# Performance work log

Measured on AMD Instinct MI355X. Metric: run time of the kernel, lower is better.

The kernel has to match this reference:

```python
import jax, jax.numpy as jnp
import numpy as np

# Config mirrors CrossAttentionAudio2T(dim=768, n_head=12, num_frames=16, spec_frames=8,
# attn_all_frame=True, audio_patch=196, time_encoding=False, use_stpos=True)
B, T, N, NA, ST, D, H = 4, 8, 196, 196, 8, 768, 12
HD = D // H
SCALE = HD ** -0.5


def setup_inputs() -> dict:
    key = jax.random.key(0)
    ks = jax.random.split(key, 12)
    r = lambda k, s: jax.random.normal(k, s, dtype=jnp.float32)
    return dict(
        t_x=r(ks[0], (B, T * N, D)),
        audio=r(ks[1], (NA + 2, B * ST, D)),
        vmae_space_pos=SCALE * r(ks[2], (N, D)),
        audio_space_pos=SCALE * r(ks[3], (NA, D)),
        vmae_temporal_pos=SCALE * r(ks[4], (T, D)),
        audio_temporal_pos=SCALE * r(ks[5], (ST, D)),
        q_w=0.02 * r(ks[6], (D, D)),
        q_b=jnp.zeros((D,), jnp.float32),
        kv_w=0.02 * r(ks[7], (2 * D, D)),
        kv_b=jnp.zeros((2 * D,), jnp.float32),
        proj_w=0.02 * r(ks[8], (D, D)),
        proj_b=jnp.zeros((D,), jnp.float32),
    )


def reference(t_x, audio, vmae_space_pos, audio_space_pos, vmae_temporal_pos,
              audio_temporal_pos, q_w, q_b, kv_w, kv_b, proj_w, proj_b):
    # --- video query tokens: add spatial + temporal pos embeds ---
    x = t_x.reshape(B, T, N, D) + vmae_space_pos          # [B,T,N,D] + [N,D]
    x = x.transpose(0, 2, 1, 3) + vmae_temporal_pos       # [B,N,T,D] + [T,D]
    x = x.transpose(0, 2, 1, 3).reshape(B, T * N, D)      # 'b n t d -> b (t n) d'

    # --- audio key/value tokens: drop 2 lead tokens, add pos embeds ---
    a = audio[2:].reshape(NA, B, ST, D).transpose(1, 2, 0, 3)  # 'n (b t) d -> b t n d'
    a = a + audio_space_pos                                    # [B,ST,NA,D] + [NA,D]
    a = a.transpose(0, 2, 1, 3) + audio_temporal_pos           # [B,NA,ST,D] + [ST,D]
    a = a.reshape(B, NA * ST, D)                               # 'b n t d -> b (n t) d'

    # --- projections ---
    q = (x @ q_w.T + q_b).reshape(B, T * N, H, HD).transpose(0, 2, 1, 3)   # [B,H,Lq,HD]
    kv = (a @ kv_w.T + kv_b).reshape(B, NA * ST, 2, H, HD)
    k = kv[:, :, 0].transpose(0, 2, 1, 3)                                  # [B,H,Lk,HD]
    v = kv[:, :, 1].transpose(0, 2, 1, 3)

    # --- scaled dot-product cross-attention (full score matrix, as in source) ---
    attn = jax.nn.softmax(jnp.einsum('bhqd,bhkd->bhqk', q * SCALE, k), axis=-1)
    o = jnp.einsum('bhqk,bhkd->bhqd', attn, v)
    o = o.transpose(0, 2, 1, 3).reshape(B, T * N, D)
    return o @ proj_w.T + proj_b
```

## Files before the change

### kernel.cpp

```cpp
#include <hip/hip_runtime.h>

typedef short s8v __attribute__((ext_vector_type(8)));
typedef short s4v __attribute__((ext_vector_type(4)));
typedef float f4v __attribute__((ext_vector_type(4)));

#define LQ 1568
#define LK 1568
#define NH 12
#define LQP 1664

__device__ __forceinline__ unsigned short f2bf(float f) {
  union { float f; unsigned u; } x; x.f = f;
  unsigned r = x.u + 0x7FFFu + ((x.u >> 16) & 1u);
  return (unsigned short)(r >> 16);
}
__device__ __forceinline__ float bf2f(unsigned s) {
  union { unsigned u; float f; } x; x.u = s << 16;
  return x.f;
}

__global__ void prep_all(const float* __restrict__ t_x, const float* __restrict__ audio,
                         const float* __restrict__ sp, const float* __restrict__ asp,
                         const float* __restrict__ tp, const float* __restrict__ atp,
                         const float* __restrict__ q_w, const float* __restrict__ kv_w,
                         const float* __restrict__ proj_w,
                         unsigned short* __restrict__ xb, unsigned short* __restrict__ ab,
                         unsigned short* __restrict__ wq, unsigned short* __restrict__ wkv,
                         unsigned short* __restrict__ wp, int total4) {
  const int n1 = 768 * 768 / 4, n2 = 1536 * 768 / 4;
  const int nconv = 2 * n1 + n2;
  int i = blockIdx.x * 256 + threadIdx.x;
  if (i < nconv) {
    const float* src; unsigned short* dst; int j = i;
    if (i < n1)           { src = q_w;    dst = wq;  }
    else if (i < n1 + n2) { src = kv_w;   dst = wkv; j = i - n1; }
    else                  { src = proj_w; dst = wp;  j = i - n1 - n2; }
    float4 v = *(const float4*)(src + (size_t)j * 4);
    ushort4 o;
    o.x = f2bf(v.x); o.y = f2bf(v.y); o.z = f2bf(v.z); o.w = f2bf(v.w);
    *(ushort4*)(dst + (size_t)j * 4) = o;
    return;
  }
  i -= nconv;
  if (i >= 2 * total4) return;
  if (i < total4) {
    int d4 = (i % 192) * 4;
    int row = i / 192;
    int l = row % LQ;
    int t = l / 196, n = l % 196;
    float4 a  = *(const float4*)(t_x + (size_t)i * 4);
    float4 s  = *(const float4*)(sp + n * 768 + d4);
    float4 tt = *(const float4*)(tp + t * 768 + d4);
    ushort4 o;
    o.x = f2bf(a.x + s.x + tt.x);
    o.y = f2bf(a.y + s.y + tt.y);
    o.z = f2bf(a.z + s.z + tt.z);
    o.w = f2bf(a.w + s.w + tt.w);
    *(ushort4*)(xb + (size_t)i * 4) = o;
  } else {
    i -= total4;
    int d4 = (i % 192) * 4;
    int row = i / 192;
    int b = row / LK;
    int r2 = row % LK;
    int na = r2 >> 3, ta = r2 & 7;
    const float* src = audio + ((size_t)(2 + na) * 32 + b * 8 + ta) * 768 + d4;
    float4 a  = *(const float4*)src;
    float4 s  = *(const float4*)(asp + na * 768 + d4);
    float4 tt = *(const float4*)(atp + ta * 768 + d4);
    ushort4 o;
    o.x = f2bf(a.x + s.x + tt.x);
    o.y = f2bf(a.y + s.y + tt.y);
    o.z = f2bf(a.z + s.z + tt.z);
    o.w = f2bf(a.w + s.w + tt.w);
    *(ushort4*)(ab + (size_t)i * 4) = o;
  }
}

__global__ __launch_bounds__(256, 4) void gemm_qkv(
    const unsigned short* __restrict__ xb, const unsigned short* __restrict__ ab,
    const unsigned short* __restrict__ wq, const unsigned short* __restrict__ wkv,
    const float* __restrict__ q_b, const float* __restrict__ kv_b,
    unsigned short* __restrict__ Qs, unsigned short* __restrict__ Kb,
    unsigned short* __restrict__ Vb) {
  __shared__ __align__(16) unsigned short sm[128 * 136];
  unsigned short* As = sm;
  unsigned short* Bs = sm + 8192;
  const int tid = threadIdx.x;
  const int lane = tid & 63, wave = tid >> 6;
  const int wm = wave & 1, wn = wave >> 1;
  const int l15 = lane & 15, quad = lane >> 4;
  const int lr = tid >> 3, lc = (tid & 7) * 8;
  const int row0 = blockIdx.x * 128;
  const int y = blockIdx.y;
  const bool isQ = (y < 6);
  const int col0 = (isQ ? y : y - 6) * 128;
  const unsigned short* A = isQ ? xb : ab;
  const unsigned short* W = isQ ? wq : wkv;
  const float* bias = isQ ? q_b : kv_b;

  f4v acc[4][4] = {};
  for (int k0 = 0; k0 < 768; k0 += 64) {
    __syncthreads();
#pragma unroll
    for (int it = 0; it < 4; ++it) {
      int row = lr + it * 32;
      __builtin_amdgcn_global_load_lds(
          (const __attribute__((address_space(1))) unsigned int*)(A + (size_t)(row0 + row) * 768 + k0 + lc),
          (__attribute__((address_space(3))) unsigned int*)(As + row * 64 + lc), 16, 0, 0);
      __builtin_amdgcn_global_load_lds(
          (const __attribute__((address_space(1))) unsigned int*)(W + (size_t)(col0 + row) * 768 + k0 + lc),
          (__attribute__((address_space(3))) unsigned int*)(Bs + row * 64 + lc), 16, 0, 0);
    }
    __syncthreads();
#pragma unroll
    for (int kk = 0; kk < 2; ++kk) {
      s8v af[4], bf[4];
#pragma unroll
      for (int i = 0; i < 4; ++i) {
        af[i] = *(const s8v*)(As + (wm * 64 + i * 16 + l15) * 64 + kk * 32 + quad * 8);
        bf[i] = *(const s8v*)(Bs + (wn * 64 + i * 16 + l15) * 64 + kk * 32 + quad * 8);
      }
#pragma unroll
      for (int mi = 0; mi < 4; ++mi)
#pragma unroll
        for (int ni = 0; ni < 4; ++ni)
          acc[mi][ni] = __builtin_amdgcn_mfma_f32_16x16x32_bf16(af[mi], bf[ni],
                                                               acc[mi][ni], 0, 0, 0);
    }
  }

  if (!isQ && col0 >= 768) {
#pragma unroll
    for (int mi = 0; mi < 4; ++mi) {
      int rowg = row0 + wm * 64 + mi * 16 + quad * 4;
#pragma unroll
      for (int ni = 0; ni < 4; ++ni) {
        int colg = col0 + wn * 64 + ni * 16 + l15;
        float bv = bias[colg];
        int oo = colg - 768;
        int h = oo >> 6, hd = oo & 63;
        int b = rowg / LK, l0 = rowg - b * LK;
        ushort4 pk;
        pk.x = f2bf(acc[mi][ni][0] + bv);
        pk.y = f2bf(acc[mi][ni][1] + bv);
        pk.z = f2bf(acc[mi][ni][2] + bv);
        pk.w = f2bf(acc[mi][ni][3] + bv);
        *(ushort4*)(Vb + ((((size_t)b * NH + h) * 392 + (l0 >> 2)) * 64 + hd) * 4) = pk;
      }
    }
    return;
  }

  const float sc = isQ ? 0.18033688011112042f : 1.0f;
  __syncthreads();
#pragma unroll
  for (int mi = 0; mi < 4; ++mi) {
    int rl = wm * 64 + mi * 16 + quad * 4;
#pragma unroll
    for (int ni = 0; ni < 4; ++ni) {
      int cl = wn * 64 + ni * 16 + l15;
      float bv = bias[col0 + cl];
#pragma unroll
      for (int r = 0; r < 4; ++r)
        sm[(rl + r) * 136 + cl] = f2bf((acc[mi][ni][r] + bv) * sc);
    }
  }
  __syncthreads();
  {
    int row = tid >> 1, half = tid & 1;
    int gl = row0 + row;
    int b = gl / LQ, l = gl - b * LQ;
    const unsigned short* src = sm + row * 136 + half * 64;
    unsigned short* dst;
    if (isQ) {
      dst = Qs + (((size_t)b * NH + (col0 >> 6) + half) * LQ + l) * 64;
    } else {
      int h = (col0 >> 6) + half;
      int tile = l / 112, rr = l - tile * 112;
      dst = Kb + (((size_t)b * NH + h) * 14 + tile) * 8064 + rr * 72;
    }
#pragma unroll
    for (int j = 0; j < 8; ++j)
      *(uint4*)(dst + j * 8) = *(const uint4*)(src + j * 8);
  }
}

__global__ __launch_bounds__(256, 4) void gemm_proj(
    const unsigned short* __restrict__ A, const unsigned short* __restrict__ W,
    const float* __restrict__ bias, float* __restrict__ out) {
  __shared__ __align__(16) unsigned short As[64 * 64];
  __shared__ __align__(16) unsigned short Bs[128 * 64];
  const int tid = threadIdx.x;
  const int lane = tid & 63, wave = tid >> 6;
  const int wm = wave & 1, wn = wave >> 1;
  const int l15 = lane & 15, quad = lane >> 4;
  const int row0 = blockIdx.x * 64;
  const int col0 = blockIdx.y * 128;
  const int lr = tid >> 3, lc = (tid & 7) * 8;

  f4v acc[2][4] = {};
  for (int k0 = 0; k0 < 768; k0 += 64) {
    __syncthreads();
#pragma unroll
    for (int it = 0; it < 2; ++it) {
      int row = lr + it * 32;
      __builtin_amdgcn_global_load_lds(
          (const __attribute__((address_space(1))) unsigned int*)(A + (size_t)(row0 + row) * 768 + k0 + lc),
          (__attribute__((address_space(3))) unsigned int*)(As + row * 64 + lc), 16, 0, 0);
    }
#pragma unroll
    for (int it = 0; it < 4; ++it) {
      int row = lr + it * 32;
      __builtin_amdgcn_global_load_lds(
          (const __attribute__((address_space(1))) unsigned int*)(W + (size_t)(col0 + row) * 768 + k0 + lc),
          (__attribute__((address_space(3))) unsigned int*)(Bs + row * 64 + lc), 16, 0, 0);
    }
    __syncthreads();
#pragma unroll
    for (int kk = 0; kk < 2; ++kk) {
      s8v af[2], bf[4];
#pragma unroll
      for (int i = 0; i < 2; ++i)
        af[i] = *(const s8v*)(As + (wm * 32 + i * 16 + l15) * 64 + kk * 32 + quad * 8);
#pragma unroll
      for (int i = 0; i < 4; ++i)
        bf[i] = *(const s8v*)(Bs + (wn * 64 + i * 16 + l15) * 64 + kk * 32 + quad * 8);
#pragma unroll
      for (int mi = 0; mi < 2; ++mi)
#pragma unroll
        for (int ni = 0; ni < 4; ++ni)
          acc[mi][ni] = __builtin_amdgcn_mfma_f32_16x16x32_bf16(af[mi], bf[ni],
                                                               acc[mi][ni], 0, 0, 0);
    }
  }

#pragma unroll
  for (int mi = 0; mi < 2; ++mi) {
    int rowg = row0 + wm * 32 + mi * 16 + quad * 4;
#pragma unroll
    for (int ni = 0; ni < 4; ++ni) {
      int colg = col0 + wn * 64 + ni * 16 + l15;
      float bv = bias[colg];
#pragma unroll
      for (int r = 0; r < 4; ++r)
        out[(size_t)(rowg + r) * 768 + colg] = acc[mi][ni][r] + bv;
    }
  }
}

__global__ __launch_bounds__(256, 4) void attn(
    const unsigned short* __restrict__ Q, const unsigned short* __restrict__ Kg,
    const unsigned short* __restrict__ Vsw,
    unsigned short* __restrict__ Op, float* __restrict__ Lp, int Z) {
  __shared__ __align__(16) unsigned short Kl[112 * 72];
  __shared__ __align__(16) unsigned short Vl[112 * 64];
  const int tid = threadIdx.x;
  const int lane = tid & 63, wave = tid >> 6;
  const int l15 = lane & 15, quad = lane >> 4;
  const int bh = blockIdx.y;
  const int q0 = blockIdx.x * 128;
  const int z = blockIdx.z;
  const int t0 = (z * 14) / Z, t1 = ((z + 1) * 14) / Z;
  const size_t base = (size_t)bh * LK * 64;

  s8v qf[2][2];
#pragma unroll
  for (int mt = 0; mt < 2; ++mt)
#pragma unroll
    for (int kk = 0; kk < 2; ++kk) {
      int row = q0 + wave * 32 + mt * 16 + l15;
      if (row > LQ - 1) row = LQ - 1;
      qf[mt][kk] = *(const s8v*)(Q + base + (size_t)row * 64 + kk * 32 + quad * 8);
    }

  f4v of[2][4] = {};
  float lr[2] = {0.0f, 0.0f};

  for (int kt = t0; kt < t1; ++kt) {
    __syncthreads();
    const unsigned short* Ksrc = Kg + ((size_t)bh * 14 + kt) * 8064;
    for (int c = tid; c < 1008; c += 256)
      __builtin_amdgcn_global_load_lds(
          (const __attribute__((address_space(1))) unsigned int*)(Ksrc + c * 8),
          (__attribute__((address_space(3))) unsigned int*)(Kl + c * 8), 16, 0, 0);
    const unsigned short* Vsrc = Vsw + base + (size_t)kt * 112 * 64;
    for (int c = tid; c < 896; c += 256)
      __builtin_amdgcn_global_load_lds(
          (const __attribute__((address_space(1))) unsigned int*)(Vsrc + c * 8),
          (__attribute__((address_space(3))) unsigned int*)(Vl + c * 8), 16, 0, 0);
    __syncthreads();

#pragma unroll
    for (int nt = 0; nt < 7; ++nt) {
      s8v kf0 = *(const s8v*)(Kl + (nt * 16 + l15) * 72 + quad * 8);
      s8v kf1 = *(const s8v*)(Kl + (nt * 16 + l15) * 72 + 32 + quad * 8);
      s4v pf[2];
#pragma unroll
      for (int mt = 0; mt < 2; ++mt) {
        f4v s = {};
        s = __builtin_amdgcn_mfma_f32_16x16x32_bf16(kf0, qf[mt][0], s, 0, 0, 0);
        s = __builtin_amdgcn_mfma_f32_16x16x32_bf16(kf1, qf[mt][1], s, 0, 0, 0);
        float p0 = __builtin_amdgcn_exp2f(s[0]);
        float p1 = __builtin_amdgcn_exp2f(s[1]);
        float p2 = __builtin_amdgcn_exp2f(s[2]);
        float p3 = __builtin_amdgcn_exp2f(s[3]);
        lr[mt] += (p0 + p1) + (p2 + p3);
        union { float f; unsigned u; } a0, a1, a2, a3;
        a0.f = p0; a1.f = p1; a2.f = p2; a3.f = p3;
        union { uint2 u; s4v s; } pk;
        pk.u.x = __builtin_amdgcn_perm(a1.u, a0.u, 0x07060302u);
        pk.u.y = __builtin_amdgcn_perm(a3.u, a2.u, 0x07060302u);
        pf[mt] = pk.s;
      }
#pragma unroll
      for (int nd = 0; nd < 4; ++nd) {
        s4v vf = *(const s4v*)(Vl + ((nt * 4 + quad) << 8) + ((nd * 16 + l15) << 2));
        of[0][nd] = __builtin_amdgcn_mfma_f32_16x16x16bf16_1k(pf[0], vf, of[0][nd], 0, 0, 0);
        of[1][nd] = __builtin_amdgcn_mfma_f32_16x16x16bf16_1k(pf[1], vf, of[1][nd], 0, 0, 0);
      }
    }
  }

#pragma unroll
  for (int mt = 0; mt < 2; ++mt) {
    lr[mt] += __shfl_xor(lr[mt], 16);
    lr[mt] += __shfl_xor(lr[mt], 32);
  }

  const size_t bbase = (((size_t)z * 48 + bh) * 13 + blockIdx.x) * 8192;
#pragma unroll
  for (int mt = 0; mt < 2; ++mt) {
#pragma unroll
    for (int nd = 0; nd < 4; ++nd) {
      union { uint2 u; ushort4 s; } pk;
      pk.s.x = f2bf(of[mt][nd][0]);
      pk.s.y = f2bf(of[mt][nd][1]);
      pk.s.z = f2bf(of[mt][nd][2]);
      pk.s.w = f2bf(of[mt][nd][3]);
      *(uint2*)(Op + bbase + (size_t)(((wave * 2 + mt) * 4 + nd) * 256 + lane * 4)) = pk.u;
    }
    if (quad == 0)
      Lp[((size_t)z * 48 + bh) * LQP + q0 + wave * 32 + mt * 16 + l15] = lr[mt];
  }
}

__global__ void attn_merge(const unsigned short* __restrict__ Op,
                           const float* __restrict__ Lp,
                           unsigned short* __restrict__ Om, int Z) {
  int i = blockIdx.x * 256 + threadIdx.x;
  int c = i & 2047;
  int t = i >> 11;
  int x = t % 13, bh = t / 13;
  int lane = c & 63, fo = c >> 6;
  int nd = fo & 3, wm = fo >> 2;
  int quad = lane >> 4, l15 = lane & 15;
  int rowl = (wm >> 1) * 32 + (wm & 1) * 16 + quad * 4;
  int col = nd * 16 + l15;
  float acc[4] = {};
  float ls[4] = {};
  for (int z = 0; z < Z; ++z) {
    size_t zb = (size_t)z * 48 + bh;
    uint2 v = *(const uint2*)(Op + (zb * 13 + x) * 8192 + (size_t)c * 4);
    acc[0] += bf2f(v.x & 0xffffu); acc[1] += bf2f(v.x >> 16);
    acc[2] += bf2f(v.y & 0xffffu); acc[3] += bf2f(v.y >> 16);
    float4 lv = *(const float4*)(Lp + zb * LQP + x * 128 + rowl);
    ls[0] += lv.x; ls[1] += lv.y; ls[2] += lv.z; ls[3] += lv.w;
  }
  int b = bh / NH, h = bh - b * NH;
#pragma unroll
  for (int r = 0; r < 4; ++r) {
    int l = x * 128 + rowl + r;
    if (l >= LQ) continue;
    Om[((size_t)b * LQ + l) * 768 + h * 64 + col] = f2bf(acc[r] / ls[r]);
  }
}

extern "C" void kernel_launch(void* const* d_in, const int* in_sizes, int n_in,
                              void* d_out, int out_size, void* d_ws, size_t ws_size,
                              hipStream_t stream) {
  const float* t_x    = (const float*)d_in[0];
  const float* audio  = (const float*)d_in[1];
  const float* sp     = (const float*)d_in[2];
  const float* asp    = (const float*)d_in[3];
  const float* tp     = (const float*)d_in[4];
  const float* atp    = (const float*)d_in[5];
  const float* q_w    = (const float*)d_in[6];
  const float* q_b    = (const float*)d_in[7];
  const float* kv_w   = (const float*)d_in[8];
  const float* kv_b   = (const float*)d_in[9];
  const float* proj_w = (const float*)d_in[10];
  const float* proj_b = (const float*)d_in[11];
  float* out = (float*)d_out;

  char* ws = (char*)d_ws;
  size_t off = 0;
  auto alloc = [&](size_t bytes) -> void* {
    void* p = ws + off;
    off += (bytes + 255) & ~(size_t)255;
    return p;
  };
  const size_t TOK = 6272;
  unsigned short* xb  = (unsigned short*)alloc(TOK * 768 * 2);
  unsigned short* ab  = (unsigned short*)alloc(TOK * 768 * 2);
  unsigned short* wq  = (unsigned short*)alloc(768 * 768 * 2);
  unsigned short* wkv = (unsigned short*)alloc(1536 * 768 * 2);
  unsigned short* wp  = (unsigned short*)alloc(768 * 768 * 2);
  unsigned short* Qs  = (unsigned short*)alloc(TOK * 768 * 2);
  unsigned short* Kb  = (unsigned short*)alloc((size_t)48 * 14 * 8064 * 2);
  unsigned short* Vb  = (unsigned short*)alloc(TOK * 768 * 2);

  auto need = [&](int Zq) {
    return off + (size_t)Zq * 48 * 13 * 8192 * 2 + (size_t)Zq * 48 * LQP * 4 + 512;
  };
  int Z;
  unsigned short *Op, *Om;
  float* Lp;
  if (ws_size >= need(4)) {
    Z = 4;
    Op = (unsigned short*)alloc((size_t)4 * 48 * 13 * 8192 * 2);
    Lp = (float*)alloc((size_t)4 * 48 * LQP * 4);
  } else {
    Z = 2;
    Op = (unsigned short*)ws;
    Lp = (float*)(ws + (size_t)2 * 48 * 13 * 8192 * 2);
  }
  Om = Qs;

  dim3 blk(256);
  const int n1 = 768 * 768 / 4, n2 = 1536 * 768 / 4;
  int total4 = (int)(TOK * 192);
  int nprep = 2 * n1 + n2 + 2 * total4;
  prep_all<<<dim3((nprep + 255) / 256), blk, 0, stream>>>(
      t_x, audio, sp, asp, tp, atp, q_w, kv_w, proj_w, xb, ab, wq, wkv, wp, total4);

  gemm_qkv<<<dim3(49, 18), blk, 0, stream>>>(xb, ab, wq, wkv, q_b, kv_b, Qs, Kb, Vb);

  attn<<<dim3(13, 48, Z), blk, 0, stream>>>(Qs, Kb, Vb, Op, Lp, Z);

  attn_merge<<<dim3(48 * 13 * 2048 / 256), blk, 0, stream>>>(Op, Lp, Om, Z);

  gemm_proj<<<dim3(98, 6), blk, 0, stream>>>(Om, wp, proj_b, out);
}
```

Measured before the change: 229.0 us.

## Double attention query tile per block and remap grid for XCD locality

Each attention block now processes 256 query rows (64 per wave) instead of 128, so every K/V tile staged in LDS feeds twice as many MFMAs and per-block load and sync overhead is amortized. The grid is flattened to 1D and remapped so that blocks sharing the same (batch*head, split) land on the same XCD, improving L2 reuse of K/V. Launch bounds drop to 3 blocks per CU to allow more registers for the larger accumulator set, and a Z=3 workspace fallback is added. The risk is lower occupancy, more padded rows (1792 vs 1664), and fewer blocks to fill the GPU.

```diff
diff --git a/kernel.cpp b/kernel.cpp
--- a/kernel.cpp
+++ b/kernel.cpp
@@ -7,7 +7,7 @@
 #define LQ 1568
 #define LK 1568
 #define NH 12
-#define LQP 1664
+#define LQP2 1792
 
 __device__ __forceinline__ unsigned short f2bf(float f) {
   union { float f; unsigned u; } x; x.f = f;
@@ -249,7 +249,7 @@
   }
 }
 
-__global__ __launch_bounds__(256, 4) void attn(
+__global__ __launch_bounds__(256, 3) void attn(
     const unsigned short* __restrict__ Q, const unsigned short* __restrict__ Kg,
     const unsigned short* __restrict__ Vsw,
     unsigned short* __restrict__ Op, float* __restrict__ Lp, int Z) {
@@ -258,24 +258,30 @@
   const int tid = threadIdx.x;
   const int lane = tid & 63, wave = tid >> 6;
   const int l15 = lane & 15, quad = lane >> 4;
-  const int bh = blockIdx.y;
-  const int q0 = blockIdx.x * 128;
-  const int z = blockIdx.z;
+  const int id = blockIdx.x;
+  const int xcd = id & 7;
+  const int j = id >> 3;
+  const int x = j % 7;
+  const int p = j / 7;
+  const int pair = xcd * 6 * Z + p;
+  const int bh = pair / Z;
+  const int z = pair % Z;
+  const int q0 = x * 256;
   const int t0 = (z * 14) / Z, t1 = ((z + 1) * 14) / Z;
   const size_t base = (size_t)bh * LK * 64;
 
-  s8v qf[2][2];
-#pragma unroll
-  for (int mt = 0; mt < 2; ++mt)
+  s8v qf[4][2];
+#pragma unroll
+  for (int mt = 0; mt < 4; ++mt)
 #pragma unroll
     for (int kk = 0; kk < 2; ++kk) {
-      int row = q0 + wave * 32 + mt * 16 + l15;
+      int row = q0 + wave * 64 + mt * 16 + l15;
       if (row > LQ - 1) row = LQ - 1;
       qf[mt][kk] = *(const s8v*)(Q + base + (size_t)row * 64 + kk * 32 + quad * 8);
     }
 
-  f4v of[2][4] = {};
-  float lr[2] = {0.0f, 0.0f};
+  f4v of[4][4] = {};
+  float lr[4] = {0.0f, 0.0f, 0.0f, 0.0f};
 
   for (int kt = t0; kt < t1; ++kt) {
     __syncthreads();
@@ -295,9 +301,9 @@
     for (int nt = 0; nt < 7; ++nt) {
       s8v kf0 = *(const s8v*)(Kl + (nt * 16 + l15) * 72 + quad * 8);
       s8v kf1 = *(const s8v*)(Kl + (nt * 16 + l15) * 72 + 32 + quad * 8);
-      s4v pf[2];
-#pragma unroll
-      for (int mt = 0; mt < 2; ++mt) {
+      s4v pf[4];
+#pragma unroll
+      for (int mt = 0; mt < 4; ++mt) {
         f4v s = {};
         s = __builtin_amdgcn_mfma_f32_16x16x32_bf16(kf0, qf[mt][0], s, 0, 0, 0);
         s = __builtin_amdgcn_mfma_f32_16x16x32_bf16(kf1, qf[mt][1], s, 0, 0, 0);
@@ -316,21 +322,22 @@
 #pragma unroll
       for (int nd = 0; nd < 4; ++nd) {
         s4v vf = *(const s4v*)(Vl + ((nt * 4 + quad) << 8) + ((nd * 16 + l15) << 2));
-        of[0][nd] = __builtin_amdgcn_mfma_f32_16x16x16bf16_1k(pf[0], vf, of[0][nd], 0, 0, 0);
-        of[1][nd] = __builtin_amdgcn_mfma_f32_16x16x16bf16_1k(pf[1], vf, of[1][nd], 0, 0, 0);
+#pragma unroll
+        for (int mt = 0; mt < 4; ++mt)
+          of[mt][nd] = __builtin_amdgcn_mfma_f32_16x16x16bf16_1k(pf[mt], vf, of[mt][nd], 0, 0, 0);
       }
     }
   }
 
 #pragma unroll
-  for (int mt = 0; mt < 2; ++mt) {
+  for (int mt = 0; mt < 4; ++mt) {
     lr[mt] += __shfl_xor(lr[mt], 16);
     lr[mt] += __shfl_xor(lr[mt], 32);
   }
 
-  const size_t bbase = (((size_t)z * 48 + bh) * 13 + blockIdx.x) * 8192;
-#pragma unroll
-  for (int mt = 0; mt < 2; ++mt) {
+  const size_t bbase = (((size_t)z * 48 + bh) * 7 + x) * 16384;
+#pragma unroll
+  for (int mt = 0; mt < 4; ++mt) {
 #pragma unroll
     for (int nd = 0; nd < 4; ++nd) {
       union { uint2 u; ushort4 s; } pk;
@@ -338,10 +345,10 @@
       pk.s.y = f2bf(of[mt][nd][1]);
       pk.s.z = f2bf(of[mt][nd][2]);
       pk.s.w = f2bf(of[mt][nd][3]);
-      *(uint2*)(Op + bbase + (size_t)(((wave * 2 + mt) * 4 + nd) * 256 + lane * 4)) = pk.u;
+      *(uint2*)(Op + bbase + (size_t)(((wave * 4 + mt) * 4 + nd) * 256 + lane * 4)) = pk.u;
     }
     if (quad == 0)
-      Lp[((size_t)z * 48 + bh) * LQP + q0 + wave * 32 + mt * 16 + l15] = lr[mt];
+      Lp[((size_t)z * 48 + bh) * LQP2 + q0 + wave * 64 + mt * 16 + l15] = lr[mt];
   }
 }
 
@@ -349,28 +356,28 @@
                            const float* __restrict__ Lp,
                            unsigned short* __restrict__ Om, int Z) {
   int i = blockIdx.x * 256 + threadIdx.x;
-  int c = i & 2047;
-  int t = i >> 11;
-  int x = t % 13, bh = t / 13;
+  int c = i & 4095;
+  int t = i >> 12;
+  int x = t % 7, bh = t / 7;
   int lane = c & 63, fo = c >> 6;
-  int nd = fo & 3, wm = fo >> 2;
+  int nd = fo & 3, wmt = fo >> 2;
   int quad = lane >> 4, l15 = lane & 15;
-  int rowl = (wm >> 1) * 32 + (wm & 1) * 16 + quad * 4;
+  int rowl = (wmt >> 2) * 64 + (wmt & 3) * 16 + quad * 4;
   int col = nd * 16 + l15;
   float acc[4] = {};
   float ls[4] = {};
   for (int z = 0; z < Z; ++z) {
     size_t zb = (size_t)z * 48 + bh;
-    uint2 v = *(const uint2*)(Op + (zb * 13 + x) * 8192 + (size_t)c * 4);
+    uint2 v = *(const uint2*)(Op + (zb * 7 + x) * 16384 + (size_t)c * 4);
     acc[0] += bf2f(v.x & 0xffffu); acc[1] += bf2f(v.x >> 16);
     acc[2] += bf2f(v.y & 0xffffu); acc[3] += bf2f(v.y >> 16);
-    float4 lv = *(const float4*)(Lp + zb * LQP + x * 128 + rowl);
+    float4 lv = *(const float4*)(Lp + zb * LQP2 + x * 256 + rowl);
     ls[0] += lv.x; ls[1] += lv.y; ls[2] += lv.z; ls[3] += lv.w;
   }
   int b = bh / NH, h = bh - b * NH;
 #pragma unroll
   for (int r = 0; r < 4; ++r) {
-    int l = x * 128 + rowl + r;
+    int l = x * 256 + rowl + r;
     if (l >= LQ) continue;
     Om[((size_t)b * LQ + l) * 768 + h * 64 + col] = f2bf(acc[r] / ls[r]);
   }
@@ -410,20 +417,24 @@
   unsigned short* Kb  = (unsigned short*)alloc((size_t)48 * 14 * 8064 * 2);
   unsigned short* Vb  = (unsigned short*)alloc(TOK * 768 * 2);
 
-  auto need = [&](int Zq) {
-    return off + (size_t)Zq * 48 * 13 * 8192 * 2 + (size_t)Zq * 48 * LQP * 4 + 512;
-  };
+  const size_t opz = (size_t)48 * 7 * 16384 * 2;
+  const size_t lpz = (size_t)48 * LQP2 * 4;
+  auto need = [&](int Zq) { return off + (size_t)Zq * (opz + lpz) + 1024; };
   int Z;
   unsigned short *Op, *Om;
   float* Lp;
   if (ws_size >= need(4)) {
     Z = 4;
-    Op = (unsigned short*)alloc((size_t)4 * 48 * 13 * 8192 * 2);
-    Lp = (float*)alloc((size_t)4 * 48 * LQP * 4);
+    Op = (unsigned short*)alloc(4 * opz);
+    Lp = (float*)alloc(4 * lpz);
+  } else if (ws_size >= need(3)) {
+    Z = 3;
+    Op = (unsigned short*)alloc(3 * opz);
+    Lp = (float*)alloc(3 * lpz);
   } else {
     Z = 2;
     Op = (unsigned short*)ws;
-    Lp = (float*)(ws + (size_t)2 * 48 * 13 * 8192 * 2);
+    Lp = (float*)(ws + 2 * opz);
   }
   Om = Qs;
 
@@ -436,9 +447,9 @@
 
   gemm_qkv<<<dim3(49, 18), blk, 0, stream>>>(xb, ab, wq, wkv, q_b, kv_b, Qs, Kb, Vb);
 
-  attn<<<dim3(13, 48, Z), blk, 0, stream>>>(Qs, Kb, Vb, Op, Lp, Z);
-
-  attn_merge<<<dim3(48 * 13 * 2048 / 256), blk, 0, stream>>>(Op, Lp, Om, Z);
+  attn<<<dim3(7 * 48 * Z), blk, 0, stream>>>(Qs, Kb, Vb, Op, Lp, Z);
+
+  attn_merge<<<dim3(48 * 7 * 4096 / 256), blk, 0, stream>>>(Op, Lp, Om, Z);
 
   gemm_proj<<<dim3(98, 6), blk, 0, stream>>>(Om, wp, proj_b, out);
 }
```

Result: slower. 342.3 us (+49.5%).
